# Kernel optimization log

Hardware: AMD Instinct MI355X
Metric: run time of the kernel (lower is better)

The kernel has to match this reference:

```python
import jax, jax.numpy as jnp
import numpy as np

MASK_ID = 3
MAX_SEN = 128
SEN_DIM = 128
EMBED = 1024


def setup_inputs() -> dict:
    key = jax.random.key(0)
    ks = jax.random.split(key, 12)
    B, S, E, D = 8, 8192, EMBED, SEN_DIM
    s = 0.02
    return {
        "input_ids": jax.random.randint(ks[0], (B, S), 0, 64),
        "hidden_states": jax.random.normal(ks[1], (B, S, E), jnp.float32),
        "Wv": jax.random.normal(ks[2], (E, D), jnp.float32) * s,
        "bv": jnp.zeros((D,), jnp.float32),
        "Wq": jax.random.normal(ks[3], (E, D), jnp.float32) * s,
        "bq": jnp.zeros((D,), jnp.float32),
        "Wk": jax.random.normal(ks[4], (D, D), jnp.float32) * s,
        "bk": jnp.zeros((D,), jnp.float32),
        "Wvt": jax.random.normal(ks[5], (D, D), jnp.float32) * s,
        "bvt": jnp.zeros((D,), jnp.float32),
        "Wo": jax.random.normal(ks[6], (D, E), jnp.float32) * s,
        "bo": jnp.zeros((E,), jnp.float32),
    }


def reference(input_ids, hidden_states, Wv, bv, Wq, bq, Wk, bk, Wvt, bvt, Wo, bo):
    B, S, E = hidden_states.shape
    dt = hidden_states.dtype

    # sentence segmentation: each mask token t with running count c belongs to bucket c-1
    mask = input_ids == MASK_ID                               # (B, S)
    csum = jnp.cumsum(mask.astype(jnp.int32), axis=1)         # (B, S)
    # tokens that are not mask tokens (or overflow max_sen_num) go to dummy bucket MAX_SEN
    seg = jnp.where(mask & (csum <= MAX_SEN), csum - 1, MAX_SEN)  # (B, S)

    # segment-sum replacement for torch.bmm(sen_pos_mask, hidden_states)
    b_idx = jnp.arange(B)[:, None]
    pooled = jnp.zeros((B, MAX_SEN + 1, E), dt).at[b_idx, seg].add(hidden_states)[:, :MAX_SEN]  # (B, M, E)

    static_sen_states = pooled @ Wv + bv                      # (B, M, 128)

    q_token = (hidden_states @ Wq + bq) * (SEN_DIM ** -0.5)   # (B, S, 128)
    k_sen = static_sen_states @ Wk + bk                       # (B, M, 128)
    v_sen = static_sen_states @ Wvt + bvt                     # (B, M, 128)

    # token t may attend to sentences 0..csum[t]-1
    tmp_mask = (jnp.arange(MAX_SEN)[None, None, :] + 1) <= csum[:, :, None]  # (B, S, M)
    neg = jnp.finfo(dt).min
    logits = jnp.einsum('bsd,bmd->bsm', q_token, k_sen) + jnp.where(tmp_mask, jnp.zeros((), dt), neg)
    attn = jax.nn.softmax(logits, axis=-1) * tmp_mask.astype(dt)  # (B, S, M)

    sen_attn_output = jnp.einsum('bsm,bmd->bsd', attn, v_sen) @ Wo + bo  # (B, S, E)
    return sen_attn_output
```

## Files before the change

### kernel.cpp

```cpp
#include <hip/hip_runtime.h>
#include <hip/hip_bf16.h>

#define MASK_ID 3
#define MAX_SEN 128
#define NB 8
#define SEQ 8192
#define EMB 1024
#define DIM 128

typedef __attribute__((ext_vector_type(8))) short short8v;
typedef __attribute__((ext_vector_type(4))) float f32x4;

#define MFMA(a, b, c) __builtin_amdgcn_mfma_f32_16x16x32_bf16(a, b, c, 0, 0, 0)

__device__ __forceinline__ short f2b(float x) {
    union { float f; unsigned u; } v; v.f = x;
    unsigned r = (v.u + 0x7FFFu + ((v.u >> 16) & 1u)) >> 16;
    return (short)r;
}

__device__ __forceinline__ unsigned cvtpk(float a, float b) {
    unsigned r;
    asm("v_cvt_pk_bf16_f32 %0, %1, %2" : "=v"(r) : "v"(a), "v"(b));
    return r;
}

__device__ __forceinline__ short8v pack8(float4 a, float4 b) {
    union { short8v s; unsigned u[4]; } r;
    r.u[0] = cvtpk(a.x, a.y);
    r.u[1] = cvtpk(a.z, a.w);
    r.u[2] = cvtpk(b.x, b.y);
    r.u[3] = cvtpk(b.z, b.w);
    return r.s;
}

__global__ __launch_bounds__(1024) void seg_kernel(const int* __restrict__ ids,
                                                   int* __restrict__ pos,
                                                   int* __restrict__ nvis) {
    int b = blockIdx.x;
    int tid = threadIdx.x;
    __shared__ int sc[1024];
    __shared__ int sc2[1024];
    const int PER = SEQ / 1024;
    int base = b * SEQ + tid * PER;

    int ids_l[PER];
    int cnt = 0;
    #pragma unroll
    for (int j = 0; j < PER; j++) {
        ids_l[j] = ids[base + j];
        cnt += (ids_l[j] == MASK_ID) ? 1 : 0;
    }
    if (tid < MAX_SEN) pos[b * MAX_SEN + tid] = -1;
    sc[tid] = cnt;
    __syncthreads();

    int* src = sc;
    int* dst = sc2;
    for (int off = 1; off < 1024; off <<= 1) {
        int v = src[tid];
        if (tid >= off) v += src[tid - off];
        dst[tid] = v;
        __syncthreads();
        int* t = src; src = dst; dst = t;
    }
    int incl = src[tid];
    int run = incl - cnt;

    #pragma unroll
    for (int j = 0; j < PER; j++) {
        if (ids_l[j] == MASK_ID) {
            run++;
            if (run <= MAX_SEN) pos[b * MAX_SEN + run - 1] = tid * PER + j;
        }
        int nv = run; if (nv > MAX_SEN) nv = MAX_SEN;
        nvis[base + j] = nv;
    }
}

__global__ __launch_bounds__(256) void prep_w(const float* __restrict__ Wq,
                                              const float* __restrict__ Wo,
                                              short* __restrict__ WqTt,
                                              short* __restrict__ WoTt) {
    int idx = blockIdx.x * 256 + threadIdx.x;
    {
        int e = idx >> 7, d = idx & 127;
        int c = e >> 6, ks = (e >> 5) & 1, lq = (e >> 3) & 3, j = e & 7;
        int cf = d >> 4, lr = d & 15;
        WqTt[(((c * 2 + ks) * 8 + cf) * 512) + (lq * 16 + lr) * 8 + j] = f2b(Wq[idx]);
    }
    {
        int dd = idx >> 10, e = idx & 1023;
        int ef = e >> 4, lr = e & 15;
        int kk = dd >> 5, lq = (dd >> 3) & 3, j = dd & 7;
        WoTt[((ef * 4 + kk) * 512) + (lq * 16 + lr) * 8 + j] = f2b(Wo[idx]);
    }
}

__global__ __launch_bounds__(128) void statkv_kernel(const float* __restrict__ hidden,
                                                     const float* __restrict__ Wv, const float* __restrict__ bv,
                                                     const float* __restrict__ Wk, const float* __restrict__ bk,
                                                     const float* __restrict__ Wvt, const float* __restrict__ bvt,
                                                     const int* __restrict__ pos,
                                                     short* __restrict__ k_t, short* __restrict__ vT_t) {
    int m = blockIdx.x, b = blockIdx.y;
    int d = threadIdx.x;
    __shared__ float h[EMB];
    __shared__ float srow[DIM];
    int p = pos[b * MAX_SEN + m];
    float acc = bv[d];
    if (p >= 0) {
        const float* hp = hidden + ((size_t)b * SEQ + p) * EMB;
        for (int e = d; e < EMB; e += 128) h[e] = hp[e];
        __syncthreads();
        float a0 = 0.f, a1 = 0.f, a2 = 0.f, a3 = 0.f;
        for (int e = 0; e < EMB; e += 4) {
            a0 += h[e]     * Wv[e * DIM + d];
            a1 += h[e + 1] * Wv[(e + 1) * DIM + d];
            a2 += h[e + 2] * Wv[(e + 2) * DIM + d];
            a3 += h[e + 3] * Wv[(e + 3) * DIM + d];
        }
        acc += (a0 + a1) + (a2 + a3);
    }
    srow[d] = acc;
    __syncthreads();
    float k0 = 0.f, k1 = 0.f, v0 = 0.f, v1 = 0.f;
    for (int e = 0; e < DIM; e += 2) {
        float s0 = srow[e], s1 = srow[e + 1];
        k0 += s0 * Wk[e * DIM + d];
        k1 += s1 * Wk[(e + 1) * DIM + d];
        v0 += s0 * Wvt[e * DIM + d];
        v1 += s1 * Wvt[(e + 1) * DIM + d];
    }
    {
        int kk = d >> 5, lq = (d >> 3) & 3, j = d & 7;
        int fid = (m >> 4) * 4 + kk;
        k_t[(b << 14) + fid * 512 + (lq * 16 + (m & 15)) * 8 + j] = f2b(bk[d] + k0 + k1);
    }
    {
        int df = d >> 4, kk = m >> 5, lq = (m >> 3) & 3, j = m & 7;
        int fid = df * 4 + kk;
        vT_t[(b << 14) + fid * 512 + (lq * 16 + (d & 15)) * 8 + j] = f2b(bvt[d] + v0 + v1);
    }
}

__global__ __launch_bounds__(256, 3) void attn_kernel(
    const float* __restrict__ hidden,
    const short* __restrict__ WqTt, const float* __restrict__ bq,
    const short* __restrict__ k_t, const short* __restrict__ vT_t,
    const short* __restrict__ WoTt, const float* __restrict__ bo,
    const int* __restrict__ nvis,
    float* __restrict__ out) {
    int wg = (blockIdx.x & 7) * 128 + (blockIdx.x >> 3);
    int b  = wg >> 7;
    int s0 = (wg & 127) * 64;
    int tid = threadIdx.x;
    int lane = tid & 63;
    int w  = tid >> 6;
    int lr = lane & 15;
    int lq = lane >> 4;

    __shared__ __align__(16) char SH[49152];
    char* Ab  = SH;
    char* pPc = SH;
    char* odc = SH + 16384;
    char* qPc = SH + 32768;

    const size_t hrow = (size_t)b * SEQ + s0;
    f32x4 zero = {0.f, 0.f, 0.f, 0.f};

    f32x4 acc[4][2];
    #pragma unroll
    for (int rf = 0; rf < 4; rf++) { acc[rf][0] = zero; acc[rf][1] = zero; }

    int G0 = tid * 2, row0 = G0 >> 3, kq0 = G0 & 7;
    int G1 = G0 + 1,  row1 = G1 >> 3, kq1 = G1 & 7;
    const float* ha0 = hidden + (hrow + row0) * EMB + kq0 * 8;
    const float* ha1 = hidden + (hrow + row1) * EMB + kq1 * 8;
    int dst0 = (row0 * 128 + kq0 * 16) ^ ((row0 & 7) << 4);
    int dst1 = (row1 * 128 + kq1 * 16) ^ ((row1 & 7) << 4);

    float4 pa0[4], pa1[4], pa2[4];
    short8v Wa[4], Wb[4];

#define LOADA(C, PA) do { \
    PA[0] = *(const float4*)(ha0 + (C) * 64); \
    PA[1] = *(const float4*)(ha0 + (C) * 64 + 4); \
    PA[2] = *(const float4*)(ha1 + (C) * 64); \
    PA[3] = *(const float4*)(ha1 + (C) * 64 + 4); } while (0)

#define LOADW(C, W) do { \
    const short* wp = WqTt + ((C) * 16 + 2 * w) * 512 + lane * 8; \
    W[0] = *(const short8v*)(wp); \
    W[1] = *(const short8v*)(wp + 512); \
    W[2] = *(const short8v*)(wp + 8 * 512); \
    W[3] = *(const short8v*)(wp + 9 * 512); } while (0)

#define STORE_A(PA) do { \
    *(short8v*)(Ab + dst0) = pack8(PA[0], PA[1]); \
    *(short8v*)(Ab + dst1) = pack8(PA[2], PA[3]); } while (0)

#define COMPUTE(W) do { \
    _Pragma("unroll") \
    for (int ks = 0; ks < 2; ks++) { \
        _Pragma("unroll") \
        for (int rf = 0; rf < 4; rf++) { \
            int row = rf * 16 + lr; \
            short8v fa = *(short8v*)(Ab + ((row * 128 + ks * 64 + lq * 16) ^ ((row & 7) << 4))); \
            acc[rf][0] = MFMA(fa, W[ks * 2 + 0], acc[rf][0]); \
            acc[rf][1] = MFMA(fa, W[ks * 2 + 1], acc[rf][1]); \
        } } } while (0)

#define ITER(c, PA, WW, DO_A, DO_W) do { \
    __builtin_amdgcn_s_barrier();                  \
    STORE_A(PA);                                   \
    if (DO_A) LOADA((c) + 3, PA); \
    asm volatile("s_waitcnt lgkmcnt(0)" ::: "memory"); \
    __builtin_amdgcn_sched_barrier(0); \
    __builtin_amdgcn_s_barrier();                  \
    COMPUTE(WW); \
    if (DO_W) LOADW((c) + 2, WW);                  \
    } while (0)

    LOADW(0, Wa);
    LOADW(1, Wb);
    LOADA(0, pa0);
    LOADA(1, pa1);
    LOADA(2, pa2);

    ITER(0,  pa0, Wa, 1, 1);
    ITER(1,  pa1, Wb, 1, 1);
    ITER(2,  pa2, Wa, 1, 1);
    ITER(3,  pa0, Wb, 1, 1);
    ITER(4,  pa1, Wa, 1, 1);
    ITER(5,  pa2, Wb, 1, 1);
    ITER(6,  pa0, Wa, 1, 1);
    ITER(7,  pa1, Wb, 1, 1);
    ITER(8,  pa2, Wa, 1, 1);
    ITER(9,  pa0, Wb, 1, 1);
    ITER(10, pa1, Wa, 1, 1);
    ITER(11, pa2, Wb, 1, 1);
    ITER(12, pa0, Wa, 1, 1);
    ITER(13, pa1, Wb, 0, 1);
    ITER(14, pa2, Wa, 0, 0);
    ITER(15, pa0, Wb, 0, 0);

    {
        const float scale = 0.08838834764831845f;
        int d0 = w * 32 + lr;
        float bq0 = bq[d0], bq1 = bq[d0 + 16];
        #pragma unroll
        for (int rf = 0; rf < 4; rf++)
            #pragma unroll
            for (int r = 0; r < 4; r++) {
                int row = rf * 16 + lq * 4 + r;
                int x = (row & 7) << 4;
                *(short*)(qPc + row * 256 + ((d0 * 2) ^ x))        = f2b((acc[rf][0][r] + bq0) * scale);
                *(short*)(qPc + row * 256 + (((d0 + 16) * 2) ^ x)) = f2b((acc[rf][1][r] + bq1) * scale);
            }
    }
    __syncthreads();

    {
        f32x4 l[4][2];
        #pragma unroll
        for (int rf = 0; rf < 4; rf++) { l[rf][0] = zero; l[rf][1] = zero; }
        const short* kbase = k_t + (b << 14) + (2 * w) * 4 * 512 + lane * 8;
        #pragma unroll
        for (int kk = 0; kk < 4; kk++) {
            const short8v fb0 = *(const short8v*)(kbase + kk * 512);
            const short8v fb1 = *(const short8v*)(kbase + (4 + kk) * 512);
            #pragma unroll
            for (int rf = 0; rf < 4; rf++) {
                int row = rf * 16 + lr;
                int x = (row & 7) << 4;
                short8v fa = *(short8v*)(qPc + row * 256 + ((kk * 64 + lq * 16) ^ x));
                l[rf][0] = MFMA(fa, fb0, l[rf][0]);
                l[rf][1] = MFMA(fa, fb1, l[rf][1]);
            }
        }
        #pragma unroll
        for (int rf = 0; rf < 4; rf++)
            #pragma unroll
            for (int r = 0; r < 4; r++) {
                int row = rf * 16 + lq * 4 + r;
                int x = (row & 7) << 4;
                *(float*)(SH + row * 512 + (((w * 32 + lr) * 4) ^ x))      = l[rf][0][r];
                *(float*)(SH + row * 512 + (((w * 32 + 16 + lr) * 4) ^ x)) = l[rf][1][r];
            }
    }
    __syncthreads();

    {
        int t = tid >> 2, sub = tid & 3;
        int nv = nvis[b * SEQ + s0 + t];
        int x = (t & 7) << 4;
        float pv[32];
        #pragma unroll
        for (int u = 0; u < 8; u++) {
            float4 v = *(const float4*)(SH + t * 512 + ((sub * 128 + u * 16) ^ x));
            pv[u * 4]     = v.x; pv[u * 4 + 1] = v.y;
            pv[u * 4 + 2] = v.z; pv[u * 4 + 3] = v.w;
        }
        int base_m = sub * 32;
        float mx = -3.0e38f;
        #pragma unroll
        for (int i = 0; i < 32; i++)
            mx = (base_m + i < nv) ? fmaxf(mx, pv[i]) : mx;
        mx = fmaxf(mx, __shfl_xor(mx, 1));
        mx = fmaxf(mx, __shfl_xor(mx, 2));
        float sum = 0.f;
        #pragma unroll
        for (int i = 0; i < 32; i++) {
            float e = (base_m + i < nv) ? __expf(pv[i] - mx) : 0.f;
            pv[i] = e;
            sum += e;
        }
        sum += __shfl_xor(sum, 1);
        sum += __shfl_xor(sum, 2);
        float inv = (nv > 0) ? 1.0f / sum : 0.f;

        __syncthreads();

        #pragma unroll
        for (int u = 0; u < 4; u++) {
            union { short8v s; unsigned uu[4]; } p;
            #pragma unroll
            for (int i = 0; i < 4; i++)
                p.uu[i] = cvtpk(pv[u * 8 + 2 * i] * inv, pv[u * 8 + 2 * i + 1] * inv);
            *(short8v*)(pPc + t * 256 + ((sub * 64 + u * 16) ^ x)) = p.s;
        }
    }
    __syncthreads();

    {
        f32x4 o[4][2];
        #pragma unroll
        for (int rf = 0; rf < 4; rf++) { o[rf][0] = zero; o[rf][1] = zero; }
        const short* vbase = vT_t + (b << 14) + (2 * w) * 4 * 512 + lane * 8;
        #pragma unroll
        for (int kk = 0; kk < 4; kk++) {
            const short8v fb0 = *(const short8v*)(vbase + kk * 512);
            const short8v fb1 = *(const short8v*)(vbase + (4 + kk) * 512);
            #pragma unroll
            for (int rf = 0; rf < 4; rf++) {
                int row = rf * 16 + lr;
                int x = (row & 7) << 4;
                short8v fa = *(short8v*)(pPc + row * 256 + ((kk * 64 + lq * 16) ^ x));
                o[rf][0] = MFMA(fa, fb0, o[rf][0]);
                o[rf][1] = MFMA(fa, fb1, o[rf][1]);
            }
        }
        int d0 = w * 32 + lr;
        #pragma unroll
        for (int rf = 0; rf < 4; rf++)
            #pragma unroll
            for (int r = 0; r < 4; r++) {
                int row = rf * 16 + lq * 4 + r;
                int x = (row & 7) << 4;
                *(short*)(odc + row * 256 + ((d0 * 2) ^ x))        = f2b(o[rf][0][r]);
                *(short*)(odc + row * 256 + (((d0 + 16) * 2) ^ x)) = f2b(o[rf][1][r]);
            }
    }
    __syncthreads();

    {
        short8v af[4][4];
        #pragma unroll
        for (int rf = 0; rf < 4; rf++)
            #pragma unroll
            for (int kk = 0; kk < 4; kk++) {
                int row = rf * 16 + lr;
                int x = (row & 7) << 4;
                af[rf][kk] = *(short8v*)(odc + row * 256 + ((kk * 64 + lq * 16) ^ x));
            }
        #pragma unroll
        for (int grp = 0; grp < 4; grp++) {
            int colbase = w * 256 + grp * 64;
            f32x4 ac[4][4];
            #pragma unroll
            for (int rf = 0; rf < 4; rf++)
                #pragma unroll
                for (int cf = 0; cf < 4; cf++) ac[rf][cf] = zero;
            #pragma unroll
            for (int kk = 0; kk < 4; kk++) {
                #pragma unroll
                for (int cf = 0; cf < 4; cf++) {
                    const short8v bb = *(const short8v*)(WoTt
                        + ((w * 16 + grp * 4 + cf) * 4 + kk) * 512 + lane * 8);
                    #pragma unroll
                    for (int rf = 0; rf < 4; rf++)
                        ac[rf][cf] = MFMA(af[rf][kk], bb, ac[rf][cf]);
                }
            }
            #pragma unroll
            for (int cf = 0; cf < 4; cf++) {
                int col = colbase + cf * 16 + lr;
                float bov = bo[col];
                #pragma unroll
                for (int rf = 0; rf < 4; rf++)
                    #pragma unroll
                    for (int r = 0; r < 4; r++)
                        out[(hrow + rf * 16 + lq * 4 + r) * EMB + col] = ac[rf][cf][r] + bov;
            }
        }
    }
}

extern "C" void kernel_launch(void* const* d_in, const int* in_sizes, int n_in,
                              void* d_out, int out_size, void* d_ws, size_t ws_size,
                              hipStream_t stream) {
    const int*   ids    = (const int*)d_in[0];
    const float* hidden = (const float*)d_in[1];
    const float* Wv     = (const float*)d_in[2];
    const float* bv     = (const float*)d_in[3];
    const float* Wq     = (const float*)d_in[4];
    const float* bq     = (const float*)d_in[5];
    const float* Wk     = (const float*)d_in[6];
    const float* bk     = (const float*)d_in[7];
    const float* Wvt    = (const float*)d_in[8];
    const float* bvt    = (const float*)d_in[9];
    const float* Wo     = (const float*)d_in[10];
    const float* bo     = (const float*)d_in[11];

    char* ws = (char*)d_ws;
    int*   pos   = (int*)ws;
    int*   nvis  = (int*)(ws + (4 << 10));
    short* k_t   = (short*)(ws + (260 << 10));
    short* vT_t  = (short*)(ws + (516 << 10));
    short* WqTt  = (short*)(ws + (772 << 10));
    short* WoTt  = (short*)(ws + (1028 << 10));

    seg_kernel<<<NB, 1024, 0, stream>>>(ids, pos, nvis);
    prep_w<<<512, 256, 0, stream>>>(Wq, Wo, WqTt, WoTt);
    dim3 g2(MAX_SEN, NB);
    statkv_kernel<<<g2, 128, 0, stream>>>(hidden, Wv, bv, Wk, bk, Wvt, bvt, pos, k_t, vT_t);
    attn_kernel<<<NB * (SEQ / 64), 256, 0, stream>>>(hidden, WqTt, bq, k_t, vT_t, WoTt, bo,
                                                     nvis, (float*)d_out);
}
```

Before: 228.7 us.

## Batch sentence rows in statkv, vectorize weight prep, deepen attention A prefetch

The statkv kernel now handles four sentences per block, so each Wv/Wk/Wvt load is reused across four rows instead of one, and the grid shrinks accordingly. prep_w now has each thread build a full 8-element bf16 fragment and write it as one vector store, using an eighth as many blocks. The attention kernel's hidden-state prefetch grows from three to five register buffers, loading five chunks ahead to hide more global latency. The cost is more registers per thread in attn_kernel under its 3-waves occupancy bound, which may cause spills or lower occupancy.

```diff
diff --git a/kernel.cpp b/kernel.cpp
--- a/kernel.cpp
+++ b/kernel.cpp
@@ -82,18 +82,26 @@
                                               const float* __restrict__ Wo,
                                               short* __restrict__ WqTt,
                                               short* __restrict__ WoTt) {
-    int idx = blockIdx.x * 256 + threadIdx.x;
-    {
-        int e = idx >> 7, d = idx & 127;
-        int c = e >> 6, ks = (e >> 5) & 1, lq = (e >> 3) & 3, j = e & 7;
-        int cf = d >> 4, lr = d & 15;
-        WqTt[(((c * 2 + ks) * 8 + cf) * 512) + (lq * 16 + lr) * 8 + j] = f2b(Wq[idx]);
-    }
-    {
-        int dd = idx >> 10, e = idx & 1023;
-        int ef = e >> 4, lr = e & 15;
-        int kk = dd >> 5, lq = (dd >> 3) & 3, j = dd & 7;
-        WoTt[((ef * 4 + kk) * 512) + (lq * 16 + lr) * 8 + j] = f2b(Wo[idx]);
+    int t = blockIdx.x * 256 + threadIdx.x;
+    {
+        int fid = t >> 6, lp = t & 63;
+        int c = fid >> 4, ks = (fid >> 3) & 1, cf = fid & 7;
+        int e0 = c * 64 + ks * 32 + (lp >> 4) * 8;
+        int d = cf * 16 + (lp & 15);
+        short8v v;
+        #pragma unroll
+        for (int j = 0; j < 8; j++) v[j] = f2b(Wq[(size_t)(e0 + j) * 128 + d]);
+        *(short8v*)(WqTt + fid * 512 + lp * 8) = v;
+    }
+    {
+        int fid = t >> 6, lp = t & 63;
+        int ef = fid >> 2, kk = fid & 3;
+        int e = ef * 16 + (lp & 15);
+        int dd0 = kk * 32 + (lp >> 4) * 8;
+        short8v v;
+        #pragma unroll
+        for (int j = 0; j < 8; j++) v[j] = f2b(Wo[(size_t)(dd0 + j) * 1024 + e]);
+        *(short8v*)(WoTt + fid * 512 + lp * 8) = v;
     }
 }
 
@@ -103,44 +111,80 @@
                                                      const float* __restrict__ Wvt, const float* __restrict__ bvt,
                                                      const int* __restrict__ pos,
                                                      short* __restrict__ k_t, short* __restrict__ vT_t) {
-    int m = blockIdx.x, b = blockIdx.y;
-    int d = threadIdx.x;
-    __shared__ float h[EMB];
-    __shared__ float srow[DIM];
-    int p = pos[b * MAX_SEN + m];
-    float acc = bv[d];
-    if (p >= 0) {
-        const float* hp = hidden + ((size_t)b * SEQ + p) * EMB;
-        for (int e = d; e < EMB; e += 128) h[e] = hp[e];
-        __syncthreads();
-        float a0 = 0.f, a1 = 0.f, a2 = 0.f, a3 = 0.f;
-        for (int e = 0; e < EMB; e += 4) {
-            a0 += h[e]     * Wv[e * DIM + d];
-            a1 += h[e + 1] * Wv[(e + 1) * DIM + d];
-            a2 += h[e + 2] * Wv[(e + 2) * DIM + d];
-            a3 += h[e + 3] * Wv[(e + 3) * DIM + d];
-        }
-        acc += (a0 + a1) + (a2 + a3);
-    }
-    srow[d] = acc;
-    __syncthreads();
-    float k0 = 0.f, k1 = 0.f, v0 = 0.f, v1 = 0.f;
-    for (int e = 0; e < DIM; e += 2) {
-        float s0 = srow[e], s1 = srow[e + 1];
-        k0 += s0 * Wk[e * DIM + d];
-        k1 += s1 * Wk[(e + 1) * DIM + d];
-        v0 += s0 * Wvt[e * DIM + d];
-        v1 += s1 * Wvt[(e + 1) * DIM + d];
-    }
-    {
-        int kk = d >> 5, lq = (d >> 3) & 3, j = d & 7;
+    int mg = blockIdx.x;
+    int b  = blockIdx.y;
+    int d  = threadIdx.x;
+    __shared__ float h[4][1024];
+    __shared__ float st[4][128];
+    int m0 = mg * 4;
+
+    #pragma unroll
+    for (int j = 0; j < 4; j++) {
+        int p = pos[b * MAX_SEN + m0 + j];
+        const float* hp = hidden + ((size_t)b * SEQ + (p < 0 ? 0 : p)) * EMB;
+        #pragma unroll
+        for (int ii = 0; ii < 2; ii++) {
+            float4 v = {0.f, 0.f, 0.f, 0.f};
+            if (p >= 0) v = *(const float4*)(hp + ii * 512 + d * 4);
+            *(float4*)&h[j][ii * 512 + d * 4] = v;
+        }
+    }
+    __syncthreads();
+
+    float a0 = 0.f, a1 = 0.f, a2 = 0.f, a3 = 0.f;
+    for (int e = 0; e < 1024; e += 4) {
+        float w0 = Wv[(size_t)e * 128 + d];
+        float w1 = Wv[(size_t)(e + 1) * 128 + d];
+        float w2 = Wv[(size_t)(e + 2) * 128 + d];
+        float w3 = Wv[(size_t)(e + 3) * 128 + d];
+        float4 h0 = *(const float4*)&h[0][e];
+        float4 h1 = *(const float4*)&h[1][e];
+        float4 h2 = *(const float4*)&h[2][e];
+        float4 h3 = *(const float4*)&h[3][e];
+        a0 += h0.x * w0 + h0.y * w1 + h0.z * w2 + h0.w * w3;
+        a1 += h1.x * w0 + h1.y * w1 + h1.z * w2 + h1.w * w3;
+        a2 += h2.x * w0 + h2.y * w1 + h2.z * w2 + h2.w * w3;
+        a3 += h3.x * w0 + h3.y * w1 + h3.z * w2 + h3.w * w3;
+    }
+    float bvd = bv[d];
+    st[0][d] = bvd + a0;
+    st[1][d] = bvd + a1;
+    st[2][d] = bvd + a2;
+    st[3][d] = bvd + a3;
+    __syncthreads();
+
+    float k0 = 0.f, k1 = 0.f, k2 = 0.f, k3 = 0.f;
+    float v0 = 0.f, v1 = 0.f, v2 = 0.f, v3 = 0.f;
+    for (int e = 0; e < 128; e += 4) {
+        float wk0 = Wk[(e) * 128 + d],     wk1 = Wk[(e + 1) * 128 + d];
+        float wk2 = Wk[(e + 2) * 128 + d], wk3 = Wk[(e + 3) * 128 + d];
+        float wv0 = Wvt[(e) * 128 + d],     wv1 = Wvt[(e + 1) * 128 + d];
+        float wv2 = Wvt[(e + 2) * 128 + d], wv3 = Wvt[(e + 3) * 128 + d];
+        float4 s0 = *(const float4*)&st[0][e];
+        float4 s1 = *(const float4*)&st[1][e];
+        float4 s2 = *(const float4*)&st[2][e];
+        float4 s3 = *(const float4*)&st[3][e];
+        k0 += s0.x * wk0 + s0.y * wk1 + s0.z * wk2 + s0.w * wk3;
+        k1 += s1.x * wk0 + s1.y * wk1 + s1.z * wk2 + s1.w * wk3;
+        k2 += s2.x * wk0 + s2.y * wk1 + s2.z * wk2 + s2.w * wk3;
+        k3 += s3.x * wk0 + s3.y * wk1 + s3.z * wk2 + s3.w * wk3;
+        v0 += s0.x * wv0 + s0.y * wv1 + s0.z * wv2 + s0.w * wv3;
+        v1 += s1.x * wv0 + s1.y * wv1 + s1.z * wv2 + s1.w * wv3;
+        v2 += s2.x * wv0 + s2.y * wv1 + s2.z * wv2 + s2.w * wv3;
+        v3 += s3.x * wv0 + s3.y * wv1 + s3.z * wv2 + s3.w * wv3;
+    }
+    float kv[4] = {k0, k1, k2, k3};
+    float vv[4] = {v0, v1, v2, v3};
+    float bkd = bk[d], bvtd = bvt[d];
+    #pragma unroll
+    for (int j = 0; j < 4; j++) {
+        int m = m0 + j;
+        int kk = d >> 5, lq = (d >> 3) & 3, jj = d & 7;
         int fid = (m >> 4) * 4 + kk;
-        k_t[(b << 14) + fid * 512 + (lq * 16 + (m & 15)) * 8 + j] = f2b(bk[d] + k0 + k1);
-    }
-    {
-        int df = d >> 4, kk = m >> 5, lq = (m >> 3) & 3, j = m & 7;
-        int fid = df * 4 + kk;
-        vT_t[(b << 14) + fid * 512 + (lq * 16 + (d & 15)) * 8 + j] = f2b(bvt[d] + v0 + v1);
+        k_t[(b << 14) + fid * 512 + (lq * 16 + (m & 15)) * 8 + jj] = f2b(bkd + kv[j]);
+        int df = d >> 4, kk2 = m >> 5, lq2 = (m >> 3) & 3, j2 = m & 7;
+        int fid2 = df * 4 + kk2;
+        vT_t[(b << 14) + fid2 * 512 + (lq2 * 16 + (d & 15)) * 8 + j2] = f2b(bvtd + vv[j]);
     }
 }
 
@@ -180,7 +224,7 @@
     int dst0 = (row0 * 128 + kq0 * 16) ^ ((row0 & 7) << 4);
     int dst1 = (row1 * 128 + kq1 * 16) ^ ((row1 & 7) << 4);
 
-    float4 pa0[4], pa1[4], pa2[4];
+    float4 pa0[4], pa1[4], pa2[4], pa3[4], pa4[4];
     short8v Wa[4], Wb[4];
 
 #define LOADA(C, PA) do { \
@@ -214,7 +258,7 @@
 #define ITER(c, PA, WW, DO_A, DO_W) do { \
     __builtin_amdgcn_s_barrier();                  \
     STORE_A(PA);                                   \
-    if (DO_A) LOADA((c) + 3, PA); \
+    if (DO_A) LOADA((c) + 5, PA); \
     asm volatile("s_waitcnt lgkmcnt(0)" ::: "memory"); \
     __builtin_amdgcn_sched_barrier(0); \
     __builtin_amdgcn_s_barrier();                  \
@@ -227,22 +271,24 @@
     LOADA(0, pa0);
     LOADA(1, pa1);
     LOADA(2, pa2);
+    LOADA(3, pa3);
+    LOADA(4, pa4);
 
     ITER(0,  pa0, Wa, 1, 1);
     ITER(1,  pa1, Wb, 1, 1);
     ITER(2,  pa2, Wa, 1, 1);
-    ITER(3,  pa0, Wb, 1, 1);
-    ITER(4,  pa1, Wa, 1, 1);
-    ITER(5,  pa2, Wb, 1, 1);
-    ITER(6,  pa0, Wa, 1, 1);
-    ITER(7,  pa1, Wb, 1, 1);
-    ITER(8,  pa2, Wa, 1, 1);
-    ITER(9,  pa0, Wb, 1, 1);
-    ITER(10, pa1, Wa, 1, 1);
-    ITER(11, pa2, Wb, 1, 1);
-    ITER(12, pa0, Wa, 1, 1);
-    ITER(13, pa1, Wb, 0, 1);
-    ITER(14, pa2, Wa, 0, 0);
+    ITER(3,  pa3, Wb, 1, 1);
+    ITER(4,  pa4, Wa, 1, 1);
+    ITER(5,  pa0, Wb, 1, 1);
+    ITER(6,  pa1, Wa, 1, 1);
+    ITER(7,  pa2, Wb, 1, 1);
+    ITER(8,  pa3, Wa, 1, 1);
+    ITER(9,  pa4, Wb, 1, 1);
+    ITER(10, pa0, Wa, 1, 1);
+    ITER(11, pa1, Wb, 0, 1);
+    ITER(12, pa2, Wa, 0, 1);
+    ITER(13, pa3, Wb, 0, 1);
+    ITER(14, pa4, Wa, 0, 0);
     ITER(15, pa0, Wb, 0, 0);
 
     {
@@ -432,8 +478,8 @@
     short* WoTt  = (short*)(ws + (1028 << 10));
 
     seg_kernel<<<NB, 1024, 0, stream>>>(ids, pos, nvis);
-    prep_w<<<512, 256, 0, stream>>>(Wq, Wo, WqTt, WoTt);
-    dim3 g2(MAX_SEN, NB);
+    prep_w<<<64, 256, 0, stream>>>(Wq, Wo, WqTt, WoTt);
+    dim3 g2(32, NB);
     statkv_kernel<<<g2, 128, 0, stream>>>(hidden, Wv, bv, Wk, bk, Wvt, bvt, pos, k_t, vT_t);
     attn_kernel<<<NB * (SEQ / 64), 256, 0, stream>>>(hidden, WqTt, bq, k_t, vT_t, WoTt, bo,
                                                      nvis, (float*)d_out);
```

Result: slower. 242.2 us (+5.9%).
